# Kernel tuning notes

Hardware: AMD Instinct MI355X
Metric: run time of the kernel (lower is better)

Reference implementation:

```python
import jax, jax.numpy as jnp
import numpy as np

B, S, T, N, D, L = 8192, 10, 3, 65536, 128, 2  # batch, neigh len, node types, table size, embed_d, layers
NEG_SLOPE = 0.01  # torch LeakyReLU default


def setup_inputs() -> dict:
    key = jax.random.key(0)
    ks = jax.random.split(key, 6)
    return {
        "emb": jax.random.normal(ks[0], (T, N, D), jnp.float32) * 0.02,
        "Wih": jax.random.normal(ks[1], (L, T, D, D), jnp.float32) / np.sqrt(D).astype(np.float32),
        "Whh": jax.random.normal(ks[2], (L, T, D, D), jnp.float32) / np.sqrt(D).astype(np.float32),
        "bih": jnp.full((L, T, D), 0.1, jnp.float32),
        "bhh": jnp.full((L, T, D), 0.1, jnp.float32),
        "w_att": jax.random.normal(ks[3], (L, 2 * D), jnp.float32) / np.sqrt(2 * D).astype(np.float32),
        "ids": jax.random.randint(ks[4], (B,), 0, N),
        "neigh_idx": jax.random.randint(ks[5], (T, B, S), 0, N),
    }


def _rnn_mean(x, Wih_l, Whh_l, bih_l, bhh_l):
    """x: [T,B,S,D] neighbor embeds. torch nn.RNN(tanh): h_s = tanh(x_s@Wih^T + bih + h@Whh^T + bhh).
    Returns mean of all hidden states over time: [T,B,D]."""
    xs = jnp.moveaxis(x, 2, 0)  # [S, T, B, D]
    h0 = jnp.zeros((T, B, D), x.dtype)

    def step(h, x_s):
        h = jnp.tanh(jnp.einsum('tbd,ted->tbe', x_s, Wih_l) + bih_l[:, None, :]
                     + jnp.einsum('tbd,ted->tbe', h, Whh_l) + bhh_l[:, None, :])
        return h, h

    _, hs = jax.lax.scan(step, h0, xs)  # [S, T, B, D]
    return hs.mean(axis=0)


def reference(emb, Wih, Whh, bih, bhh, w_att, ids, neigh_idx):
    cur = emb[0][ids]  # [B, D] target node type = 0
    # per-type neighbor gather from base embedding tables (same each layer, as in source)
    neigh = jax.vmap(lambda e, i: e[i])(emb, neigh_idx)  # [T, B, S, D]
    for l in range(L):
        agg = _rnn_mean(neigh, Wih[l], Whh[l], bih[l], bhh[l])  # [T, B, D]
        cands = jnp.moveaxis(jnp.concatenate([cur[None], agg], axis=0), 0, 1)  # [B, 1+T, D]
        feat = jnp.concatenate(
            [jnp.broadcast_to(cur[:, None, :], cands.shape), cands], axis=-1)  # [B, 1+T, 2D]
        scores = feat @ w_att[l]  # [B, 1+T]
        w = jax.nn.softmax(scores, axis=1)[..., None]
        cur = jax.nn.leaky_relu(jnp.sum(w * cands, axis=1), NEG_SLOPE)
    return cur
```

## Files before the change

### kernel.cpp

```cpp
#include <hip/hip_runtime.h>
#include <hip/hip_bf16.h>

#define NB   8192
#define NS   10
#define NT   3
#define NN   65536
#define ND   128
#define NL   2
#define ROWS 32

typedef __attribute__((ext_vector_type(8))) short bf16x8;
typedef __attribute__((ext_vector_type(4))) float f32x4;

__device__ __forceinline__ unsigned int pk2(float lo, float hi) {
    unsigned int r;
    asm("v_cvt_pk_bf16_f32 %0, %1, %2" : "=v"(r) : "v"(lo), "v"(hi));
    return r;
}
__device__ __forceinline__ float fast_tanh(float x) {
    float e = __expf(2.0f * x);
    return 1.0f - __fdividef(2.0f, e + 1.0f);
}
__device__ __forceinline__ void bar_lgkm() {
    asm volatile("s_waitcnt lgkmcnt(0)\n\ts_barrier" ::: "memory");
}

__global__ __launch_bounds__(256)
void rnn_kernel(const float* __restrict__ emb, const float* __restrict__ Wih,
                const float* __restrict__ Whh, const float* __restrict__ bih,
                const float* __restrict__ bhh, const int* __restrict__ nidx,
                float* __restrict__ agg)
{
    __shared__ __align__(16) unsigned short Xs[2][ROWS * 128];
    __shared__ __align__(16) unsigned short Hs[2][ROWS * 128];

    const int bid = blockIdx.x;
    const int l   = bid / (NT * (NB / ROWS));
    const int t   = (bid / (NB / ROWS)) % NT;
    const int b0  = (bid % (NB / ROWS)) * ROWS;

    const int tid  = threadIdx.x;
    const int w    = tid >> 6;
    const int lane = tid & 63;
    const int l16  = lane & 15;
    const int lg   = lane >> 4;
    const int e0   = w * 32;
    const int rx   = l16 & 7;

    const float* Wih_lt = Wih + (size_t)(l * NT + t) * ND * ND;
    const float* Whh_lt = Whh + (size_t)(l * NT + t) * ND * ND;
    const float* bih_lt = bih + (size_t)(l * NT + t) * ND;
    const float* bhh_lt = bhh + (size_t)(l * NT + t) * ND;

    const int srow = tid >> 3;
    const int sq   = tid & 7;
    const int ssw  = srow & 7;

    const int* ip = nidx + ((size_t)t * NB + b0 + srow) * NS;
    int idxs[NS];
    #pragma unroll
    for (int s = 0; s < NS; ++s) idxs[s] = ip[s];

    float4 P[4];
    {
        const float* src = emb + ((size_t)t * NN + idxs[0]) * ND + sq * 16;
        #pragma unroll
        for (int c = 0; c < 4; ++c) P[c] = *(const float4*)(src + c * 4);
    }

    bf16x8 Af[2][8];
    #pragma unroll
    for (int mt = 0; mt < 2; ++mt) {
        #pragma unroll
        for (int kc = 0; kc < 8; ++kc) {
            const float* Wsrc = (kc < 4) ? Wih_lt : Whh_lt;
            const float* srcp = Wsrc + (size_t)(e0 + mt * 16 + l16) * ND + (kc & 3) * 32 + lg * 8;
            float4 p0 = *(const float4*)(srcp);
            float4 p1 = *(const float4*)(srcp + 4);
            int4 a;
            a.x = (int)pk2(p0.x, p0.y);
            a.y = (int)pk2(p0.z, p0.w);
            a.z = (int)pk2(p1.x, p1.y);
            a.w = (int)pk2(p1.z, p1.w);
            Af[mt][kc] = *(bf16x8*)&a;
        }
    }

    float bias[2][4];
    #pragma unroll
    for (int mt = 0; mt < 2; ++mt)
        #pragma unroll
        for (int i = 0; i < 4; ++i) {
            int e = e0 + mt * 16 + lg * 4 + i;
            bias[mt][i] = bih_lt[e] + bhh_lt[e];
        }

    f32x4 zero4; zero4[0] = 0.f; zero4[1] = 0.f; zero4[2] = 0.f; zero4[3] = 0.f;
    f32x4 Ag[2][2];
    #pragma unroll
    for (int nt = 0; nt < 2; ++nt) { Ag[nt][0] = zero4; Ag[nt][1] = zero4; }

    for (int s = 0; s < NS; ++s) {
        char* xcur = (char*)Xs[s & 1];
        char* hprv = (char*)Hs[(s + 1) & 1];
        char* hcur = (char*)Hs[s & 1];

        #pragma unroll
        for (int j = 0; j < 2; ++j) {
            int4 pk;
            pk.x = (int)pk2(P[2 * j].x,     P[2 * j].y);
            pk.y = (int)pk2(P[2 * j].z,     P[2 * j].w);
            pk.z = (int)pk2(P[2 * j + 1].x, P[2 * j + 1].y);
            pk.w = (int)pk2(P[2 * j + 1].z, P[2 * j + 1].w);
            int chunk = (2 * sq + j) ^ ssw;
            *(int4*)(xcur + srow * 256 + (chunk << 4)) = pk;
        }
        if (s + 1 < NS) {
            const float* src = emb + ((size_t)t * NN + idxs[s + 1]) * ND + sq * 16;
            #pragma unroll
            for (int c = 0; c < 4; ++c) P[c] = *(const float4*)(src + c * 4);
        }
        bar_lgkm();

        f32x4 acc[2][2];
        #pragma unroll
        for (int nt = 0; nt < 2; ++nt) { acc[nt][0] = zero4; acc[nt][1] = zero4; }

        #pragma unroll
        for (int nt = 0; nt < 2; ++nt) {
            const int r = nt * 16 + l16;
            #pragma unroll
            for (int kc = 0; kc < 8; ++kc) {
                if (kc < 4 || s > 0) {
                    const char* buf = (kc < 4) ? xcur : hprv;
                    int chunk = ((kc & 3) * 4 + lg) ^ rx;
                    bf16x8 bf = *(const bf16x8*)(buf + r * 256 + (chunk << 4));
                    acc[nt][0] = __builtin_amdgcn_mfma_f32_16x16x32_bf16(Af[0][kc], bf, acc[nt][0], 0, 0, 0);
                    acc[nt][1] = __builtin_amdgcn_mfma_f32_16x16x32_bf16(Af[1][kc], bf, acc[nt][1], 0, 0, 0);
                }
            }
        }

        #pragma unroll
        for (int nt = 0; nt < 2; ++nt) {
            const int r = nt * 16 + l16;
            const int rr = r & 7;
            #pragma unroll
            for (int mt = 0; mt < 2; ++mt) {
                f32x4 h;
                #pragma unroll
                for (int i = 0; i < 4; ++i)
                    h[i] = fast_tanh(acc[nt][mt][i] + bias[mt][i]);
                Ag[nt][mt] += h;
                int2 pk;
                pk.x = (int)pk2(h[0], h[1]);
                pk.y = (int)pk2(h[2], h[3]);
                int estart = e0 + mt * 16 + lg * 4;
                int chunk  = (estart >> 3) ^ rr;
                *(int2*)(hcur + r * 256 + (chunk << 4) + (estart & 7) * 2) = pk;
            }
        }
    }

    float* aggp = agg + ((size_t)(l * NT + t) * NB + b0) * ND;
    #pragma unroll
    for (int nt = 0; nt < 2; ++nt) {
        int b = nt * 16 + l16;
        #pragma unroll
        for (int mt = 0; mt < 2; ++mt) {
            f32x4 v = Ag[nt][mt] * 0.1f;
            *(f32x4*)(aggp + (size_t)b * ND + e0 + mt * 16 + lg * 4) = v;
        }
    }
}

__global__ __launch_bounds__(256)
void att_kernel(const float* __restrict__ emb, const int* __restrict__ ids,
                const float* __restrict__ w_att, const float* __restrict__ agg,
                float* __restrict__ cur, const int l)
{
    const int wid  = threadIdx.x >> 6;
    const int lane = threadIdx.x & 63;
    const int b    = blockIdx.x * 4 + wid;

    const float* waH  = w_att + l * 2 * ND;
    const float* waT  = waH + ND;
    const float* crow = (l == 0) ? (emb + (size_t)ids[b] * ND) : (cur + (size_t)b * ND);
    const float* ab   = agg + ((size_t)(l * NT) * NB + b) * ND;

    const float c1 = crow[lane], c2 = crow[lane + 64];
    const float h1 = waH[lane],  h2 = waH[lane + 64];
    const float t1 = waT[lane],  t2 = waT[lane + 64];
    float g1[3], g2[3];
    #pragma unroll
    for (int tt = 0; tt < 3; ++tt) {
        g1[tt] = ab[(size_t)tt * NB * ND + lane];
        g2[tt] = ab[(size_t)tt * NB * ND + lane + 64];
    }

    float dH = c1 * h1 + c2 * h2;
    float dc = c1 * t1 + c2 * t2;
    float d0 = g1[0] * t1 + g2[0] * t2;
    float d1 = g1[1] * t1 + g2[1] * t2;
    float d2 = g1[2] * t1 + g2[2] * t2;
    #pragma unroll
    for (int off = 32; off > 0; off >>= 1) {
        dH += __shfl_xor(dH, off);
        dc += __shfl_xor(dc, off);
        d0 += __shfl_xor(d0, off);
        d1 += __shfl_xor(d1, off);
        d2 += __shfl_xor(d2, off);
    }

    float s0 = dH + dc, s1 = dH + d0, s2 = dH + d1, s3 = dH + d2;
    float m  = fmaxf(fmaxf(s0, s1), fmaxf(s2, s3));
    float q0 = __expf(s0 - m), q1 = __expf(s1 - m), q2 = __expf(s2 - m), q3 = __expf(s3 - m);
    float inv = __fdividef(1.0f, q0 + q1 + q2 + q3);
    float w0 = q0 * inv, w1 = q1 * inv, w2 = q2 * inv, w3 = q3 * inv;

    float o1 = w0 * c1 + w1 * g1[0] + w2 * g1[1] + w3 * g1[2];
    float o2 = w0 * c2 + w1 * g2[0] + w2 * g2[1] + w3 * g2[2];
    o1 = (o1 > 0.f) ? o1 : 0.01f * o1;
    o2 = (o2 > 0.f) ? o2 : 0.01f * o2;

    float* orow = cur + (size_t)b * ND;
    orow[lane]      = o1;
    orow[lane + 64] = o2;
}

extern "C" void kernel_launch(void* const* d_in, const int* in_sizes, int n_in,
                              void* d_out, int out_size, void* d_ws, size_t ws_size,
                              hipStream_t stream)
{
    const float* emb  = (const float*)d_in[0];
    const float* Wih  = (const float*)d_in[1];
    const float* Whh  = (const float*)d_in[2];
    const float* bih  = (const float*)d_in[3];
    const float* bhh  = (const float*)d_in[4];
    const float* watt = (const float*)d_in[5];
    const int*   ids  = (const int*)d_in[6];
    const int*   nidx = (const int*)d_in[7];

    float* cur = (float*)d_out;
    float* agg = (float*)d_ws;

    rnn_kernel<<<dim3(NL * NT * (NB / ROWS)), dim3(256), 0, stream>>>(emb, Wih, Whh, bih, bhh, nidx, agg);
    att_kernel<<<dim3(NB / 4), dim3(256), 0, stream>>>(emb, ids, watt, agg, cur, 0);
    att_kernel<<<dim3(NB / 4), dim3(256), 0, stream>>>(emb, ids, watt, agg, cur, 1);
}
```

Baseline: 88.91 us.

## Share gathered neighbor tile across both layers in one 512-thread block

Merges the two layer-specific RNN blocks into a single 512-thread block. Each half of the waves handles one layer, and both halves read the same X tile from LDS, so the emb gather is issued once instead of twice. The change also folds the bias into the accumulator init, precomputes the LDS addresses, fully unrolls the time loop, and uses a cheaper tanh built on v_exp and v_rcp. In exchange the block is larger with more LDS and registers, which may lower occupancy, and there are half as many blocks.

```diff
diff --git a/kernel.cpp b/kernel.cpp
--- a/kernel.cpp
+++ b/kernel.cpp
@@ -17,56 +17,60 @@
     asm("v_cvt_pk_bf16_f32 %0, %1, %2" : "=v"(r) : "v"(lo), "v"(hi));
     return r;
 }
-__device__ __forceinline__ float fast_tanh(float x) {
-    float e = __expf(2.0f * x);
-    return 1.0f - __fdividef(2.0f, e + 1.0f);
+__device__ __forceinline__ float tanh_f(float x) {
+    float e, r;
+    asm("v_exp_f32 %0, %1" : "=v"(e) : "v"(x * 2.88539004f));
+    asm("v_rcp_f32 %0, %1" : "=v"(r) : "v"(e + 1.0f));
+    return fmaf(-2.0f, r, 1.0f);
 }
 __device__ __forceinline__ void bar_lgkm() {
     asm volatile("s_waitcnt lgkmcnt(0)\n\ts_barrier" ::: "memory");
 }
 
-__global__ __launch_bounds__(256)
+__global__ __launch_bounds__(512)
 void rnn_kernel(const float* __restrict__ emb, const float* __restrict__ Wih,
                 const float* __restrict__ Whh, const float* __restrict__ bih,
                 const float* __restrict__ bhh, const int* __restrict__ nidx,
                 float* __restrict__ agg)
 {
-    __shared__ __align__(16) unsigned short Xs[2][ROWS * 128];
-    __shared__ __align__(16) unsigned short Hs[2][ROWS * 128];
+    __shared__ __align__(16) char lds[6 * 8192];
 
     const int bid = blockIdx.x;
-    const int l   = bid / (NT * (NB / ROWS));
-    const int t   = (bid / (NB / ROWS)) % NT;
+    const int t   = bid / (NB / ROWS);
     const int b0  = (bid % (NB / ROWS)) * ROWS;
 
     const int tid  = threadIdx.x;
-    const int w    = tid >> 6;
+    const int wv   = tid >> 6;
+    const int lay  = wv >> 2;
     const int lane = tid & 63;
     const int l16  = lane & 15;
     const int lg   = lane >> 4;
-    const int e0   = w * 32;
+    const int e0   = (wv & 3) * 32;
     const int rx   = l16 & 7;
 
-    const float* Wih_lt = Wih + (size_t)(l * NT + t) * ND * ND;
-    const float* Whh_lt = Whh + (size_t)(l * NT + t) * ND * ND;
-    const float* bih_lt = bih + (size_t)(l * NT + t) * ND;
-    const float* bhh_lt = bhh + (size_t)(l * NT + t) * ND;
-
-    const int srow = tid >> 3;
-    const int sq   = tid & 7;
-    const int ssw  = srow & 7;
+    char* xb = lds;
+    char* hb = lds + 16384 + lay * 16384;
+
+    const int srow  = tid >> 4;
+    const int sq    = tid & 15;
+    const int xaddr = srow * 256 + ((sq ^ (srow & 7)) << 4);
 
     const int* ip = nidx + ((size_t)t * NB + b0 + srow) * NS;
     int idxs[NS];
     #pragma unroll
     for (int s = 0; s < NS; ++s) idxs[s] = ip[s];
 
-    float4 P[4];
+    float4 P0, P1;
     {
-        const float* src = emb + ((size_t)t * NN + idxs[0]) * ND + sq * 16;
-        #pragma unroll
-        for (int c = 0; c < 4; ++c) P[c] = *(const float4*)(src + c * 4);
-    }
+        const float* src = emb + ((size_t)t * NN + idxs[0]) * ND + sq * 8;
+        P0 = *(const float4*)(src);
+        P1 = *(const float4*)(src + 4);
+    }
+
+    const float* Wih_lt = Wih + (size_t)(lay * NT + t) * ND * ND;
+    const float* Whh_lt = Whh + (size_t)(lay * NT + t) * ND * ND;
+    const float* bih_lt = bih + (size_t)(lay * NT + t) * ND;
+    const float* bhh_lt = bhh + (size_t)(lay * NT + t) * ND;
 
     bf16x8 Af[2][8];
     #pragma unroll
@@ -86,13 +90,28 @@
         }
     }
 
-    float bias[2][4];
+    f32x4 biasv[2];
     #pragma unroll
     for (int mt = 0; mt < 2; ++mt)
         #pragma unroll
         for (int i = 0; i < 4; ++i) {
             int e = e0 + mt * 16 + lg * 4 + i;
-            bias[mt][i] = bih_lt[e] + bhh_lt[e];
+            biasv[mt][i] = bih_lt[e] + bhh_lt[e];
+        }
+
+    int raddr[2][4];
+    #pragma unroll
+    for (int nt = 0; nt < 2; ++nt)
+        #pragma unroll
+        for (int c = 0; c < 4; ++c)
+            raddr[nt][c] = (nt * 16 + l16) * 256 + (((c * 4 + lg) ^ rx) << 4);
+    int hwaddr[2][2];
+    #pragma unroll
+    for (int nt = 0; nt < 2; ++nt)
+        #pragma unroll
+        for (int mt = 0; mt < 2; ++mt) {
+            int es = e0 + mt * 16 + lg * 4;
+            hwaddr[nt][mt] = (nt * 16 + l16) * 256 + (((es >> 3) ^ rx) << 4) + (es & 7) * 2;
         }
 
     f32x4 zero4; zero4[0] = 0.f; zero4[1] = 0.f; zero4[2] = 0.f; zero4[3] = 0.f;
@@ -100,69 +119,63 @@
     #pragma unroll
     for (int nt = 0; nt < 2; ++nt) { Ag[nt][0] = zero4; Ag[nt][1] = zero4; }
 
+    #pragma unroll
     for (int s = 0; s < NS; ++s) {
-        char* xcur = (char*)Xs[s & 1];
-        char* hprv = (char*)Hs[(s + 1) & 1];
-        char* hcur = (char*)Hs[s & 1];
-
-        #pragma unroll
-        for (int j = 0; j < 2; ++j) {
+        {
             int4 pk;
-            pk.x = (int)pk2(P[2 * j].x,     P[2 * j].y);
-            pk.y = (int)pk2(P[2 * j].z,     P[2 * j].w);
-            pk.z = (int)pk2(P[2 * j + 1].x, P[2 * j + 1].y);
-            pk.w = (int)pk2(P[2 * j + 1].z, P[2 * j + 1].w);
-            int chunk = (2 * sq + j) ^ ssw;
-            *(int4*)(xcur + srow * 256 + (chunk << 4)) = pk;
+            pk.x = (int)pk2(P0.x, P0.y);
+            pk.y = (int)pk2(P0.z, P0.w);
+            pk.z = (int)pk2(P1.x, P1.y);
+            pk.w = (int)pk2(P1.z, P1.w);
+            *(int4*)(xb + xaddr + (s & 1) * 8192) = pk;
         }
         if (s + 1 < NS) {
-            const float* src = emb + ((size_t)t * NN + idxs[s + 1]) * ND + sq * 16;
+            const float* src = emb + ((size_t)t * NN + idxs[s + 1]) * ND + sq * 8;
+            P0 = *(const float4*)(src);
+            P1 = *(const float4*)(src + 4);
+        }
+        bar_lgkm();
+
+        f32x4 acc[2][2];
+        #pragma unroll
+        for (int nt = 0; nt < 2; ++nt) { acc[nt][0] = biasv[0]; acc[nt][1] = biasv[1]; }
+
+        #pragma unroll
+        for (int nt = 0; nt < 2; ++nt)
             #pragma unroll
-            for (int c = 0; c < 4; ++c) P[c] = *(const float4*)(src + c * 4);
-        }
-        bar_lgkm();
-
-        f32x4 acc[2][2];
-        #pragma unroll
-        for (int nt = 0; nt < 2; ++nt) { acc[nt][0] = zero4; acc[nt][1] = zero4; }
-
-        #pragma unroll
-        for (int nt = 0; nt < 2; ++nt) {
-            const int r = nt * 16 + l16;
+            for (int c = 0; c < 4; ++c) {
+                bf16x8 bf = *(const bf16x8*)(xb + raddr[nt][c] + (s & 1) * 8192);
+                acc[nt][0] = __builtin_amdgcn_mfma_f32_16x16x32_bf16(Af[0][c], bf, acc[nt][0], 0, 0, 0);
+                acc[nt][1] = __builtin_amdgcn_mfma_f32_16x16x32_bf16(Af[1][c], bf, acc[nt][1], 0, 0, 0);
+            }
+        if (s > 0) {
             #pragma unroll
-            for (int kc = 0; kc < 8; ++kc) {
-                if (kc < 4 || s > 0) {
-                    const char* buf = (kc < 4) ? xcur : hprv;
-                    int chunk = ((kc & 3) * 4 + lg) ^ rx;
-                    bf16x8 bf = *(const bf16x8*)(buf + r * 256 + (chunk << 4));
-                    acc[nt][0] = __builtin_amdgcn_mfma_f32_16x16x32_bf16(Af[0][kc], bf, acc[nt][0], 0, 0, 0);
-                    acc[nt][1] = __builtin_amdgcn_mfma_f32_16x16x32_bf16(Af[1][kc], bf, acc[nt][1], 0, 0, 0);
+            for (int nt = 0; nt < 2; ++nt)
+                #pragma unroll
+                for (int c = 0; c < 4; ++c) {
+                    bf16x8 bf = *(const bf16x8*)(hb + raddr[nt][c] + ((s + 1) & 1) * 8192);
+                    acc[nt][0] = __builtin_amdgcn_mfma_f32_16x16x32_bf16(Af[0][c + 4], bf, acc[nt][0], 0, 0, 0);
+                    acc[nt][1] = __builtin_amdgcn_mfma_f32_16x16x32_bf16(Af[1][c + 4], bf, acc[nt][1], 0, 0, 0);
                 }
-            }
-        }
-
-        #pragma unroll
-        for (int nt = 0; nt < 2; ++nt) {
-            const int r = nt * 16 + l16;
-            const int rr = r & 7;
+        }
+
+        #pragma unroll
+        for (int nt = 0; nt < 2; ++nt)
             #pragma unroll
             for (int mt = 0; mt < 2; ++mt) {
                 f32x4 h;
                 #pragma unroll
                 for (int i = 0; i < 4; ++i)
-                    h[i] = fast_tanh(acc[nt][mt][i] + bias[mt][i]);
+                    h[i] = tanh_f(acc[nt][mt][i]);
                 Ag[nt][mt] += h;
                 int2 pk;
                 pk.x = (int)pk2(h[0], h[1]);
                 pk.y = (int)pk2(h[2], h[3]);
-                int estart = e0 + mt * 16 + lg * 4;
-                int chunk  = (estart >> 3) ^ rr;
-                *(int2*)(hcur + r * 256 + (chunk << 4) + (estart & 7) * 2) = pk;
+                *(int2*)(hb + hwaddr[nt][mt] + (s & 1) * 8192) = pk;
             }
-        }
-    }
-
-    float* aggp = agg + ((size_t)(l * NT + t) * NB + b0) * ND;
+    }
+
+    float* aggp = agg + ((size_t)(lay * NT + t) * NB + b0) * ND;
     #pragma unroll
     for (int nt = 0; nt < 2; ++nt) {
         int b = nt * 16 + l16;
@@ -244,7 +257,7 @@
     float* cur = (float*)d_out;
     float* agg = (float*)d_ws;
 
-    rnn_kernel<<<dim3(NL * NT * (NB / ROWS)), dim3(256), 0, stream>>>(emb, Wih, Whh, bih, bhh, nidx, agg);
+    rnn_kernel<<<dim3(NT * (NB / ROWS)), dim3(512), 0, stream>>>(emb, Wih, Whh, bih, bhh, nidx, agg);
     att_kernel<<<dim3(NB / 4), dim3(256), 0, stream>>>(emb, ids, watt, agg, cur, 0);
     att_kernel<<<dim3(NB / 4), dim3(256), 0, stream>>>(emb, ids, watt, agg, cur, 1);
 }
```

Measured after the change: 76.20 us. 1.17x faster.
